# Performance work log

Measured on AMD Instinct MI355X. Metric: run time of the kernel, lower is better.

Reference implementation:

```python
import jax, jax.numpy as jnp
import numpy as np
import math

RANK = 2
CUTOFF = 10.0
EWALD_ALPHA = 0.3
PREFACTOR = 1.0
N_ATOMS = 100000
N_PAIRS = 2000000
BOX_L = 60.0


def _damp_factors_erfc(dr, b):
    # Ewald real-space damping factors for rank<=2 multipoles. Shape (5, P).
    u = b * dr
    erfc_u = jax.lax.erfc(u)
    exp2_u = jnp.exp(-u * u)
    u2 = u * u
    u3 = u2 * u
    u5 = u3 * u2
    u7 = u5 * u2
    p1 = jnp.zeros_like(u)
    p3 = u
    p5 = (3 * u + 2 * u3) / 3
    p7 = (15 * u + 10 * u3 + 4 * u5) / 15
    p9 = (8 * u7 + 28 * u5 + 70 * u3 + 105 * u) / 105
    pref = 2.0 / math.sqrt(math.pi)
    return jnp.stack([erfc_u + pref * p * exp2_u for p in (p1, p3, p5, p7, p9)], axis=0)


def _interaction_tensor(drVec, dampFactors, drInv):
    # Rank-2 multipole interaction tensor, shape (P, 10, 10).
    drInv2 = drInv * drInv
    drInv3 = drInv2 * drInv
    drInv5 = drInv3 * drInv2
    drVec2 = drVec * drVec
    x, y, z = drVec[:, 0], drVec[:, 1], drVec[:, 2]
    x2, y2, z2 = drVec2[:, 0], drVec2[:, 1], drVec2[:, 2]
    xy, xz, yz = x * y, x * z, y * z
    drInv7 = drInv5 * drInv2
    drInv9 = drInv7 * drInv2
    if dampFactors is not None:
        drInv = drInv * dampFactors[0]
        drInv3 = drInv3 * dampFactors[1]
        drInv5 = drInv5 * dampFactors[2]
        drInv7 = drInv7 * dampFactors[3]
        drInv9 = drInv9 * dampFactors[4]
    tx, ty, tz = -x * drInv3, -y * drInv3, -z * drInv3
    txx = 3 * x2 * drInv5 - drInv3
    txy = 3 * xy * drInv5
    txz = 3 * xz * drInv5
    tyy = 3 * y2 * drInv5 - drInv3
    tyz = 3 * yz * drInv5
    tzz = 3 * z2 * drInv5 - drInv3
    txxx = -15 * x2 * x * drInv7 + 9 * x * drInv5
    txxy = -15 * x2 * y * drInv7 + 3 * y * drInv5
    txxz = -15 * x2 * z * drInv7 + 3 * z * drInv5
    tyyy = -15 * y2 * y * drInv7 + 9 * y * drInv5
    tyyx = -15 * y2 * x * drInv7 + 3 * x * drInv5
    tyyz = -15 * y2 * z * drInv7 + 3 * z * drInv5
    tzzz = -15 * z2 * z * drInv7 + 9 * z * drInv5
    tzzx = -15 * z2 * x * drInv7 + 3 * x * drInv5
    tzzy = -15 * z2 * y * drInv7 + 3 * y * drInv5
    txyz = -15 * x * y * z * drInv7
    txxxx = 105 * x2 * x2 * drInv9 - 90 * x2 * drInv7 + 9 * drInv5
    txxxy = 105 * x2 * xy * drInv9 - 45 * xy * drInv7
    txxxz = 105 * x2 * xz * drInv9 - 45 * xz * drInv7
    txxyy = 105 * x2 * y2 * drInv9 - 15 * (x2 + y2) * drInv7 + 3 * drInv5
    txxzz = 105 * x2 * z2 * drInv9 - 15 * (x2 + z2) * drInv7 + 3 * drInv5
    txxyz = 105 * x2 * yz * drInv9 - 15 * yz * drInv7
    tyyyy = 105 * y2 * y2 * drInv9 - 90 * y2 * drInv7 + 9 * drInv5
    tyyyx = 105 * y2 * xy * drInv9 - 45 * xy * drInv7
    tyyyz = 105 * y2 * yz * drInv9 - 45 * yz * drInv7
    tyyzz = 105 * y2 * z2 * drInv9 - 15 * (y2 + z2) * drInv7 + 3 * drInv5
    tyyxz = 105 * y2 * xz * drInv9 - 15 * xz * drInv7
    tzzzz = 105 * z2 * z2 * drInv9 - 90 * z2 * drInv7 + 9 * drInv5
    tzzzx = 105 * z2 * xz * drInv9 - 45 * xz * drInv7
    tzzzy = 105 * z2 * yz * drInv9 - 45 * yz * drInv7
    tzzxy = 105 * z2 * xy * drInv9 - 15 * xy * drInv7
    rows = (drInv, -tx, -ty, -tz, txx, txy, txz, tyy, tyz, tzz,
            tx, -txx, -txy, -txz, txxx, txxy, txxz, tyyx, txyz, tzzx,
            ty, -txy, -tyy, -tyz, txxy, tyyx, txyz, tyyy, tyyz, tzzy,
            tz, -txz, -tyz, -tzz, txxz, txyz, tzzx, tyyz, tzzy, tzzz,
            txx, -txxx, -txxy, -txxz, txxxx, txxxy, txxxz, txxyy, txxyz, txxzz,
            txy, -txxy, -tyyx, -txyz, txxxy, txxyy, txxyz, tyyyx, tyyxz, tzzxy,
            txz, -txxz, -txyz, -tzzx, txxxz, txxyz, txxzz, tyyxz, tzzxy, tzzzx,
            tyy, -tyyx, -tyyy, -tyyz, txxyy, tyyyx, tyyxz, tyyyy, tyyyz, tyyzz,
            tyz, -txyz, -tyyz, -tzzy, txxyz, tyyxz, tzzxy, tyyyz, tyyzz, tzzzy,
            tzz, -tzzx, -tzzy, -tzzz, txxzz, tzzxy, tzzzx, tyyzz, tzzzy, tzzzz)
    return jnp.stack(rows, axis=-1).reshape(-1, 10, 10)


def _pack_multipoles(q, p, t):
    # [q, ux, uy, uz, Qxx, Qxy, Qxz, Qyy, Qyz, Qzz], shape (N, 10).
    cols = [q[:, None], p,
            (t[:, 0, 0] / 3)[:, None],
            ((t[:, 0, 1] + t[:, 1, 0]) / 3)[:, None],
            ((t[:, 0, 2] + t[:, 2, 0]) / 3)[:, None],
            (t[:, 1, 1] / 3)[:, None],
            ((t[:, 1, 2] + t[:, 2, 1]) / 3)[:, None],
            (t[:, 2, 2] / 3)[:, None]]
    return jnp.concatenate(cols, axis=1)


def setup_inputs() -> dict:
    key = jax.random.key(0)
    k1, k2, k3, k4, k5, k6 = jax.random.split(key, 6)
    coords = jax.random.uniform(k1, (N_ATOMS, 3), dtype=jnp.float32) * BOX_L
    box = jnp.eye(3, dtype=jnp.float32) * BOX_L
    pi = jax.random.randint(k2, (N_PAIRS,), 0, N_ATOMS)
    off = jax.random.randint(k3, (N_PAIRS,), 1, N_ATOMS)
    pj = (pi + off) % N_ATOMS  # guarantee i != j
    pairs = jnp.stack([pi, pj], axis=1).astype(jnp.int64)
    q = jax.random.normal(k4, (N_ATOMS,), dtype=jnp.float32)
    p = jax.random.normal(k5, (N_ATOMS, 3), dtype=jnp.float32)
    t = jax.random.normal(k6, (N_ATOMS, 3, 3), dtype=jnp.float32)
    return {"coords": coords, "box": box, "pairs": pairs, "q": q, "p": p, "t": t}


def reference(coords, box, pairs, q, p, t):
    box_inv = jnp.linalg.inv(box)
    dr = coords[pairs[:, 1]] - coords[pairs[:, 0]]
    # minimum-image PBC (row-vector fractional coordinates convention)
    dr_vecs = dr - jnp.round(dr @ box_inv) @ box
    dist = jnp.linalg.norm(dr_vecs, axis=1)
    mask = (dist <= CUTOFF).astype(dist.dtype)
    damps = _damp_factors_erfc(dist, EWALD_ALPHA)
    i_tensor = _interaction_tensor(dr_vecs, damps, 1.0 / dist)  # (P,10,10)
    m = _pack_multipoles(q, p, t)  # (N,10)
    ene_pairs = jnp.einsum('pa,pab,pb->p', m[pairs[:, 1]], i_tensor, m[pairs[:, 0]])
    return PREFACTOR * jnp.sum(ene_pairs * mask)
```

## Files before the change

kernel.cpp:

```cpp
#include <hip/hip_runtime.h>
#include <math.h>

#define CUTOFF2 100.0f
#define EW_ALPHA 0.3f
#define NBLOCKS 1024
#define NTHREADS 256

__global__ __launch_bounds__(NTHREADS)
void mp_pair_energy_kernel(const float* __restrict__ coords,
                           const float* __restrict__ box,
                           const int* __restrict__ pairs,
                           const float* __restrict__ q,
                           const float* __restrict__ p,
                           const float* __restrict__ t,
                           double* __restrict__ partial,
                           int n_pairs) {
    const float Lx = box[0], Ly = box[4], Lz = box[8];
    const float iLx = 1.0f / Lx, iLy = 1.0f / Ly, iLz = 1.0f / Lz;
    const float PREF = 1.1283791670955126f;

    double acc = 0.0;
    const int stride = gridDim.x * blockDim.x;
    for (int idx = blockIdx.x * blockDim.x + threadIdx.x; idx < n_pairs; idx += stride) {
        int2 pr = reinterpret_cast<const int2*>(pairs)[idx];
        int i = pr.x;
        int j = pr.y;

        float dx = coords[3*j+0] - coords[3*i+0];
        float dy = coords[3*j+1] - coords[3*i+1];
        float dz = coords[3*j+2] - coords[3*i+2];
        float x = dx - rintf(dx * iLx) * Lx;
        float y = dy - rintf(dy * iLy) * Ly;
        float z = dz - rintf(dz * iLz) * Lz;

        float r2 = x*x + y*y + z*z;
        if (r2 > CUTOFF2) continue;

        float r = sqrtf(r2);
        float rinv = 1.0f / r;

        float u  = EW_ALPHA * r;
        float u2 = u*u;
        float u3 = u2*u, u5 = u3*u2, u7 = u5*u2;
        float e2 = expf(-u2);
        float ec = erfcf(u);
        float d1 = ec;
        float d3 = ec + PREF * u * e2;
        float d5 = ec + PREF * ((3.0f*u + 2.0f*u3) * (1.0f/3.0f)) * e2;
        float d7 = ec + PREF * ((15.0f*u + 10.0f*u3 + 4.0f*u5) * (1.0f/15.0f)) * e2;
        float d9 = ec + PREF * ((105.0f*u + 70.0f*u3 + 28.0f*u5 + 8.0f*u7) * (1.0f/105.0f)) * e2;

        float ri2 = rinv * rinv;
        float r3i = rinv * ri2;
        float r5i = r3i * ri2;
        float r7i = r5i * ri2;
        float r9i = r7i * ri2;
        float R1 = rinv * d1;
        float R3 = r3i * d3;
        float R5 = r5i * d5;
        float R7 = r7i * d7;
        float R9 = r9i * d9;

        float x2 = x*x, y2 = y*y, z2 = z*z;
        float xy = x*y, xz = x*z, yz = y*z;

        float tx = -x * R3, ty = -y * R3, tz = -z * R3;
        float txx = 3.0f*x2*R5 - R3;
        float txy = 3.0f*xy*R5;
        float txz = 3.0f*xz*R5;
        float tyy = 3.0f*y2*R5 - R3;
        float tyz = 3.0f*yz*R5;
        float tzz = 3.0f*z2*R5 - R3;
        float txxx = x*(9.0f*R5 - 15.0f*x2*R7);
        float txxy = y*(3.0f*R5 - 15.0f*x2*R7);
        float txxz = z*(3.0f*R5 - 15.0f*x2*R7);
        float tyyy = y*(9.0f*R5 - 15.0f*y2*R7);
        float tyyx = x*(3.0f*R5 - 15.0f*y2*R7);
        float tyyz = z*(3.0f*R5 - 15.0f*y2*R7);
        float tzzz = z*(9.0f*R5 - 15.0f*z2*R7);
        float tzzx = x*(3.0f*R5 - 15.0f*z2*R7);
        float tzzy = y*(3.0f*R5 - 15.0f*z2*R7);
        float txyz = -15.0f*x*yz*R7;
        float txxxx = 105.0f*x2*x2*R9 - 90.0f*x2*R7 + 9.0f*R5;
        float txxxy = xy*(105.0f*x2*R9 - 45.0f*R7);
        float txxxz = xz*(105.0f*x2*R9 - 45.0f*R7);
        float txxyy = 105.0f*x2*y2*R9 - 15.0f*(x2+y2)*R7 + 3.0f*R5;
        float txxzz = 105.0f*x2*z2*R9 - 15.0f*(x2+z2)*R7 + 3.0f*R5;
        float txxyz = yz*(105.0f*x2*R9 - 15.0f*R7);
        float tyyyy = 105.0f*y2*y2*R9 - 90.0f*y2*R7 + 9.0f*R5;
        float tyyyx = xy*(105.0f*y2*R9 - 45.0f*R7);
        float tyyyz = yz*(105.0f*y2*R9 - 45.0f*R7);
        float tyyzz = 105.0f*y2*z2*R9 - 15.0f*(y2+z2)*R7 + 3.0f*R5;
        float tyyxz = xz*(105.0f*y2*R9 - 15.0f*R7);
        float tzzzz = 105.0f*z2*z2*R9 - 90.0f*z2*R7 + 9.0f*R5;
        float tzzzx = xz*(105.0f*z2*R9 - 45.0f*R7);
        float tzzzy = yz*(105.0f*z2*R9 - 45.0f*R7);
        float tzzxy = xy*(105.0f*z2*R9 - 15.0f*R7);

        const float* ti = t + 9*i;
        const float* tj = t + 9*j;
        float mi0 = q[i];
        float mi1 = p[3*i+0], mi2 = p[3*i+1], mi3 = p[3*i+2];
        float mi4 = ti[0] * (1.0f/3.0f);
        float mi5 = (ti[1] + ti[3]) * (1.0f/3.0f);
        float mi6 = (ti[2] + ti[6]) * (1.0f/3.0f);
        float mi7 = ti[4] * (1.0f/3.0f);
        float mi8 = (ti[5] + ti[7]) * (1.0f/3.0f);
        float mi9 = ti[8] * (1.0f/3.0f);
        float mj0 = q[j];
        float mj1 = p[3*j+0], mj2 = p[3*j+1], mj3 = p[3*j+2];
        float mj4 = tj[0] * (1.0f/3.0f);
        float mj5 = (tj[1] + tj[3]) * (1.0f/3.0f);
        float mj6 = (tj[2] + tj[6]) * (1.0f/3.0f);
        float mj7 = tj[4] * (1.0f/3.0f);
        float mj8 = (tj[5] + tj[7]) * (1.0f/3.0f);
        float mj9 = tj[8] * (1.0f/3.0f);

        float E0 = R1*mi0  - tx*mi1   - ty*mi2   - tz*mi3   + txx*mi4   + txy*mi5   + txz*mi6   + tyy*mi7   + tyz*mi8   + tzz*mi9;
        float E1 = tx*mi0  - txx*mi1  - txy*mi2  - txz*mi3  + txxx*mi4  + txxy*mi5  + txxz*mi6  + tyyx*mi7  + txyz*mi8  + tzzx*mi9;
        float E2 = ty*mi0  - txy*mi1  - tyy*mi2  - tyz*mi3  + txxy*mi4  + tyyx*mi5  + txyz*mi6  + tyyy*mi7  + tyyz*mi8  + tzzy*mi9;
        float E3 = tz*mi0  - txz*mi1  - tyz*mi2  - tzz*mi3  + txxz*mi4  + txyz*mi5  + tzzx*mi6  + tyyz*mi7  + tzzy*mi8  + tzzz*mi9;
        float E4 = txx*mi0 - txxx*mi1 - txxy*mi2 - txxz*mi3 + txxxx*mi4 + txxxy*mi5 + txxxz*mi6 + txxyy*mi7 + txxyz*mi8 + txxzz*mi9;
        float E5 = txy*mi0 - txxy*mi1 - tyyx*mi2 - txyz*mi3 + txxxy*mi4 + txxyy*mi5 + txxyz*mi6 + tyyyx*mi7 + tyyxz*mi8 + tzzxy*mi9;
        float E6 = txz*mi0 - txxz*mi1 - txyz*mi2 - tzzx*mi3 + txxxz*mi4 + txxyz*mi5 + txxzz*mi6 + tyyxz*mi7 + tzzxy*mi8 + tzzzx*mi9;
        float E7 = tyy*mi0 - tyyx*mi1 - tyyy*mi2 - tyyz*mi3 + txxyy*mi4 + tyyyx*mi5 + tyyxz*mi6 + tyyyy*mi7 + tyyyz*mi8 + tyyzz*mi9;
        float E8 = tyz*mi0 - txyz*mi1 - tyyz*mi2 - tzzy*mi3 + txxyz*mi4 + tyyxz*mi5 + tzzxy*mi6 + tyyyz*mi7 + tyyzz*mi8 + tzzzy*mi9;
        float E9 = tzz*mi0 - tzzx*mi1 - tzzy*mi2 - tzzz*mi3 + txxzz*mi4 + tzzxy*mi5 + tzzzx*mi6 + tyyzz*mi7 + tzzzy*mi8 + tzzzz*mi9;

        float e = mj0*E0 + mj1*E1 + mj2*E2 + mj3*E3 + mj4*E4
                + mj5*E5 + mj6*E6 + mj7*E7 + mj8*E8 + mj9*E9;

        acc += (double)e;
    }

    __shared__ double sdata[NTHREADS];
    int tid = threadIdx.x;
    sdata[tid] = acc;
    __syncthreads();
    for (int s = NTHREADS/2; s > 0; s >>= 1) {
        if (tid < s) sdata[tid] += sdata[tid + s];
        __syncthreads();
    }
    if (tid == 0) partial[blockIdx.x] = sdata[0];
}

__global__ __launch_bounds__(256)
void mp_reduce_kernel(const double* __restrict__ partial, int n, float* __restrict__ out) {
    __shared__ double sdata[256];
    int tid = threadIdx.x;
    double a = 0.0;
    for (int i = tid; i < n; i += 256) a += partial[i];
    sdata[tid] = a;
    __syncthreads();
    for (int s = 128; s > 0; s >>= 1) {
        if (tid < s) sdata[tid] += sdata[tid + s];
        __syncthreads();
    }
    if (tid == 0) out[0] = (float)sdata[0];
}

extern "C" void kernel_launch(void* const* d_in, const int* in_sizes, int n_in,
                              void* d_out, int out_size, void* d_ws, size_t ws_size,
                              hipStream_t stream) {
    const float* coords = (const float*)d_in[0];
    const float* box    = (const float*)d_in[1];
    const int*   pairs  = (const int*)d_in[2];
    const float* q      = (const float*)d_in[3];
    const float* p      = (const float*)d_in[4];
    const float* t      = (const float*)d_in[5];
    int n_pairs = in_sizes[2] / 2;

    double* partial = (double*)d_ws;

    mp_pair_energy_kernel<<<NBLOCKS, NTHREADS, 0, stream>>>(
        coords, box, pairs, q, p, t, partial, n_pairs);
    mp_reduce_kernel<<<1, 256, 0, stream>>>(partial, NBLOCKS, (float*)d_out);
}
```

Before: 36.31 us.

## Pack per-atom coords and multipoles into 64-byte AoS records for gathers

Adds a prepass kernel that packs coordinates, charge, dipole and the symmetrised quadrupole components for each atom into a 16-float aligned record. The pair kernel then fetches each atom with a few float4 loads instead of many scattered scalar loads from four arrays, cutting random-gather transactions. It also loads pairs with a nontemporal 64-bit load and doubles the grid size. The cost is an extra kernel launch that touches every atom each call, plus more workspace.

```diff
diff --git a/kernel.cpp b/kernel.cpp
--- a/kernel.cpp
+++ b/kernel.cpp
@@ -3,16 +3,35 @@
 
 #define CUTOFF2 100.0f
 #define EW_ALPHA 0.3f
-#define NBLOCKS 1024
+#define NBLOCKS 2048
 #define NTHREADS 256
+#define N_ATOMS_MAX_PAD 16
+
+__global__ __launch_bounds__(256)
+void pack_atoms_kernel(const float* __restrict__ coords,
+                       const float* __restrict__ q,
+                       const float* __restrict__ p,
+                       const float* __restrict__ t,
+                       float* __restrict__ packed,
+                       int n_atoms) {
+    int i = blockIdx.x * blockDim.x + threadIdx.x;
+    if (i >= n_atoms) return;
+    const float* ti = t + 9*i;
+    float4 a0 = make_float4(coords[3*i+0], coords[3*i+1], coords[3*i+2], q[i]);
+    float4 a1 = make_float4(p[3*i+0], p[3*i+1], p[3*i+2], ti[0] * (1.0f/3.0f));
+    float4 a2 = make_float4((ti[1] + ti[3]) * (1.0f/3.0f),
+                            (ti[2] + ti[6]) * (1.0f/3.0f),
+                            ti[4] * (1.0f/3.0f),
+                            (ti[5] + ti[7]) * (1.0f/3.0f));
+    float4 a3 = make_float4(ti[8] * (1.0f/3.0f), 0.0f, 0.0f, 0.0f);
+    float4* dst = reinterpret_cast<float4*>(packed + 16*i);
+    dst[0] = a0; dst[1] = a1; dst[2] = a2; dst[3] = a3;
+}
 
 __global__ __launch_bounds__(NTHREADS)
-void mp_pair_energy_kernel(const float* __restrict__ coords,
+void mp_pair_energy_kernel(const float* __restrict__ packed,
                            const float* __restrict__ box,
-                           const int* __restrict__ pairs,
-                           const float* __restrict__ q,
-                           const float* __restrict__ p,
-                           const float* __restrict__ t,
+                           const long long* __restrict__ pairs,
                            double* __restrict__ partial,
                            int n_pairs) {
     const float Lx = box[0], Ly = box[4], Lz = box[8];
@@ -22,13 +41,20 @@
     double acc = 0.0;
     const int stride = gridDim.x * blockDim.x;
     for (int idx = blockIdx.x * blockDim.x + threadIdx.x; idx < n_pairs; idx += stride) {
-        int2 pr = reinterpret_cast<const int2*>(pairs)[idx];
-        int i = pr.x;
-        int j = pr.y;
+        long long v = __builtin_nontemporal_load(pairs + idx);
+        int i = (int)(v & 0xffffffffLL);
+        int j = (int)(v >> 32);
 
-        float dx = coords[3*j+0] - coords[3*i+0];
-        float dy = coords[3*j+1] - coords[3*i+1];
-        float dz = coords[3*j+2] - coords[3*i+2];
+        const float4* Ai = reinterpret_cast<const float4*>(packed + 16*i);
+        const float4* Aj = reinterpret_cast<const float4*>(packed + 16*j);
+        float4 i0 = Ai[0], i1 = Ai[1], i2 = Ai[2];
+        float  mi9 = packed[16*i + 12];
+        float4 j0 = Aj[0], j1 = Aj[1], j2 = Aj[2];
+        float  mj9 = packed[16*j + 12];
+
+        float dx = j0.x - i0.x;
+        float dy = j0.y - i0.y;
+        float dz = j0.z - i0.z;
         float x = dx - rintf(dx * iLx) * Lx;
         float y = dy - rintf(dy * iLy) * Ly;
         float z = dz - rintf(dz * iLz) * Lz;
@@ -97,24 +123,14 @@
         float tzzzy = yz*(105.0f*z2*R9 - 45.0f*R7);
         float tzzxy = xy*(105.0f*z2*R9 - 15.0f*R7);
 
-        const float* ti = t + 9*i;
-        const float* tj = t + 9*j;
-        float mi0 = q[i];
-        float mi1 = p[3*i+0], mi2 = p[3*i+1], mi3 = p[3*i+2];
-        float mi4 = ti[0] * (1.0f/3.0f);
-        float mi5 = (ti[1] + ti[3]) * (1.0f/3.0f);
-        float mi6 = (ti[2] + ti[6]) * (1.0f/3.0f);
-        float mi7 = ti[4] * (1.0f/3.0f);
-        float mi8 = (ti[5] + ti[7]) * (1.0f/3.0f);
-        float mi9 = ti[8] * (1.0f/3.0f);
-        float mj0 = q[j];
-        float mj1 = p[3*j+0], mj2 = p[3*j+1], mj3 = p[3*j+2];
-        float mj4 = tj[0] * (1.0f/3.0f);
-        float mj5 = (tj[1] + tj[3]) * (1.0f/3.0f);
-        float mj6 = (tj[2] + tj[6]) * (1.0f/3.0f);
-        float mj7 = tj[4] * (1.0f/3.0f);
-        float mj8 = (tj[5] + tj[7]) * (1.0f/3.0f);
-        float mj9 = tj[8] * (1.0f/3.0f);
+        float mi0 = i0.w;
+        float mi1 = i1.x, mi2 = i1.y, mi3 = i1.z;
+        float mi4 = i1.w;
+        float mi5 = i2.x, mi6 = i2.y, mi7 = i2.z, mi8 = i2.w;
+        float mj0 = j0.w;
+        float mj1 = j1.x, mj2 = j1.y, mj3 = j1.z;
+        float mj4 = j1.w;
+        float mj5 = j2.x, mj6 = j2.y, mj7 = j2.z, mj8 = j2.w;
 
         float E0 = R1*mi0  - tx*mi1   - ty*mi2   - tz*mi3   + txx*mi4   + txy*mi5   + txz*mi6   + tyy*mi7   + tyz*mi8   + tzz*mi9;
         float E1 = tx*mi0  - txx*mi1  - txy*mi2  - txz*mi3  + txxx*mi4  + txxy*mi5  + txxz*mi6  + tyyx*mi7  + txyz*mi8  + tzzx*mi9;
@@ -169,10 +185,15 @@
     const float* p      = (const float*)d_in[4];
     const float* t      = (const float*)d_in[5];
     int n_pairs = in_sizes[2] / 2;
+    int n_atoms = in_sizes[3];
 
-    double* partial = (double*)d_ws;
+    size_t packed_bytes = (size_t)n_atoms * 16 * sizeof(float);
+    float*  packed  = (float*)d_ws;
+    double* partial = (double*)((char*)d_ws + ((packed_bytes + 255) & ~(size_t)255));
 
+    pack_atoms_kernel<<<(n_atoms + 255) / 256, 256, 0, stream>>>(
+        coords, q, p, t, packed, n_atoms);
     mp_pair_energy_kernel<<<NBLOCKS, NTHREADS, 0, stream>>>(
-        coords, box, pairs, q, p, t, partial, n_pairs);
+        packed, box, (const long long*)pairs, partial, n_pairs);
     mp_reduce_kernel<<<1, 256, 0, stream>>>(partial, NBLOCKS, (float*)d_out);
 }
```

Result: slower. 55.31 us (+52.3%).
